# Kernel tuning notes

Measured on AMD Instinct MI355X. Metric: run time of the kernel, lower is better.

The kernel has to match this reference:

```python
import jax, jax.numpy as jnp
import numpy as np

B, C, NS, NT, H = 8, 256, 16384, 8192, 8
D = C // H  # 32
EPS_ATTN = 1e-6
EPS_LN = 1e-5


def _layernorm(x, g, b):
    m = jnp.mean(x, axis=-1, keepdims=True)
    v = jnp.mean((x - m) ** 2, axis=-1, keepdims=True)
    return (x - m) * jax.lax.rsqrt(v + EPS_LN) * g + b


def setup_inputs() -> dict:
    key = jax.random.key(0)
    ks = jax.random.split(key, 16)
    s = lambda fan_in: 1.0 / np.sqrt(fan_in)
    return {
        "search_feat": jax.random.normal(ks[0], (B, C, NS), jnp.float32),
        "search_xyz": jax.random.normal(ks[1], (B, NS, 3), jnp.float32),
        "template_feat": jax.random.normal(ks[2], (B, C, NT), jnp.float32),
        "template_xyz": jax.random.normal(ks[3], (B, NT, 3), jnp.float32),
        # pos_mlp: Linear(3, C) -> ReLU -> Linear(C, C); weights stored [in, out]
        "pos_w1": jax.random.uniform(ks[4], (3, C), jnp.float32, -s(3), s(3)),
        "pos_b1": jnp.zeros((C,), jnp.float32),
        "pos_w2": jax.random.uniform(ks[5], (C, C), jnp.float32, -s(C), s(C)),
        "pos_b2": jnp.zeros((C,), jnp.float32),
        "q_w": jax.random.uniform(ks[6], (C, C), jnp.float32, -s(C), s(C)),
        "k_w": jax.random.uniform(ks[7], (C, C), jnp.float32, -s(C), s(C)),
        "v_w": jax.random.uniform(ks[8], (C, C), jnp.float32, -s(C), s(C)),
        "merge_w": jax.random.uniform(ks[9], (C, C), jnp.float32, -s(C), s(C)),
        "mlp_w1": jax.random.uniform(ks[10], (2 * C, 2 * C), jnp.float32, -s(2 * C), s(2 * C)),
        "mlp_w2": jax.random.uniform(ks[11], (2 * C, C), jnp.float32, -s(2 * C), s(2 * C)),
        "ln1_g": jnp.ones((C,), jnp.float32),
        "ln1_b": jnp.zeros((C,), jnp.float32),
        "ln2_g": jnp.ones((C,), jnp.float32),
        "ln2_b": jnp.zeros((C,), jnp.float32),
    }


def _forward(search_feat, search_xyz, template_feat, template_xyz,
             pos_w1, pos_b1, pos_w2, pos_b2, q_w, k_w, v_w, merge_w,
             mlp_w1, mlp_w2, ln1_g, ln1_b, ln2_g, ln2_b):
    bs = search_feat.shape[0]
    sf = jnp.transpose(search_feat, (0, 2, 1))     # [B, Ns, C]
    tf = jnp.transpose(template_feat, (0, 2, 1))   # [B, Nt, C]
    # positional encoding added to template features before value projection
    pos = jax.nn.relu(template_xyz @ pos_w1 + pos_b1) @ pos_w2 + pos_b2
    tfp = tf + pos
    q = (sf @ q_w).reshape(bs, -1, H, D)    # [B, Ns, H, D]
    k = (tf @ k_w).reshape(bs, -1, H, D)    # [B, Nt, H, D]
    v = (tfp @ v_w).reshape(bs, -1, H, D)   # [B, Nt, H, D]
    # linear attention with elu+1 feature map
    Q = jax.nn.elu(q) + 1.0
    K = jax.nn.elu(k) + 1.0
    v_len = v.shape[1]
    v_scaled = v / v_len
    KV = jnp.einsum('nshd,nshv->nhdv', K, v_scaled)            # [B, H, D, D]
    Z = 1.0 / (jnp.einsum('nlhd,nhd->nlh', Q, K.sum(axis=1)) + EPS_ATTN)
    msg = jnp.einsum('nlhd,nhdv,nlh->nlhv', Q, KV, Z) * v_len  # [B, Ns, H, D]
    msg = msg.reshape(bs, -1, H * D) @ merge_w
    msg = _layernorm(msg, ln1_g, ln1_b)
    msg = jax.nn.relu(jnp.concatenate([sf, msg], axis=2) @ mlp_w1) @ mlp_w2
    msg = _layernorm(msg, ln2_g, ln2_b)
    return jnp.transpose(sf + msg, (0, 2, 1))  # [B, C, Ns]


def reference(search_feat, search_xyz, template_feat, template_xyz,
              pos_w1, pos_b1, pos_w2, pos_b2, q_w, k_w, v_w, merge_w,
              mlp_w1, mlp_w2, ln1_g, ln1_b, ln2_g, ln2_b):
    return _forward(search_feat, search_xyz, template_feat, template_xyz,
                    pos_w1, pos_b1, pos_w2, pos_b2, q_w, k_w, v_w, merge_w,
                    mlp_w1, mlp_w2, ln1_g, ln1_b, ln2_g, ln2_b)
```

## Files before the change

kernel.cpp:

```cpp
#include <hip/hip_runtime.h>
#include <math.h>

#define B_  8
#define C_  256
#define NS_ 16384
#define NT_ 8192
#define H_  8
#define D_  32
#define C2_ 512
#define NCH 4
#define KVZ_ (H_*D_*D_ + H_*D_)

typedef __attribute__((ext_vector_type(8))) short bf16x8;
typedef __attribute__((ext_vector_type(4))) short bf16x4;
typedef __attribute__((ext_vector_type(4))) float f32x4;

#define PIPE_TOP(N) do {                                              \
    asm volatile("s_waitcnt vmcnt(" #N ")" ::: "memory");             \
    asm volatile("s_barrier" ::: "memory");                           \
    __builtin_amdgcn_sched_barrier(0);                                \
} while (0)
#define PIPE_BOT() do {                                               \
    __builtin_amdgcn_sched_barrier(0);                                \
    asm volatile("s_waitcnt lgkmcnt(0)" ::: "memory");                \
    asm volatile("s_barrier" ::: "memory");                           \
} while (0)

__device__ __forceinline__ short f2bf(float f) {
    unsigned u = __float_as_uint(f);
    u = (u + 0x7fffu + ((u >> 16) & 1u)) >> 16;
    return (short)u;
}
__device__ __forceinline__ float bf2f(short s) {
    return __uint_as_float(((unsigned)(unsigned short)s) << 16);
}
__device__ __forceinline__ float2 bfpair(unsigned u) {
    float2 r;
    r.x = __uint_as_float(u << 16);
    r.y = __uint_as_float(u & 0xffff0000u);
    return r;
}
__device__ __forceinline__ void load_lds16(const void* g, void* l) {
    __builtin_amdgcn_global_load_lds(
        (const __attribute__((address_space(1))) unsigned int*)g,
        (__attribute__((address_space(3))) unsigned int*)l, 16, 0, 0);
}

__global__ __launch_bounds__(256)
void castT(const float* __restrict__ in, short* __restrict__ ob, int NLEN, int b0)
{
    __shared__ float tl[32][33];
    int g = blockIdx.z, gb = b0 + g;
    int n0 = blockIdx.x * 32, c0 = blockIdx.y * 32;
    int t = threadIdx.x, tr = t >> 5, tc = t & 31;
    #pragma unroll
    for (int i = 0; i < 4; ++i)
        tl[tr + 8*i][tc] = in[((size_t)gb*C_ + c0 + tr + 8*i)*NLEN + n0 + tc];
    __syncthreads();
    #pragma unroll
    for (int i = 0; i < 4; ++i)
        ob[((size_t)g*NLEN + n0 + tr + 8*i)*C_ + c0 + tc] = f2bf(tl[tc][tr + 8*i]);
}

struct WDesc { const float* src; int K; int N; int off; int ldo; };
struct WPack { WDesc d[7]; };

__global__ __launch_bounds__(256)
void wcast_all(WPack p, short* __restrict__ wt)
{
    __shared__ float tl[32][33];
    WDesc d = p.d[blockIdx.z];
    int kt = blockIdx.x * 32, nt = blockIdx.y * 32;
    if (kt >= d.K || nt >= d.N) return;
    int t = threadIdx.x, tr = t >> 5, tc = t & 31;
    #pragma unroll
    for (int i = 0; i < 4; ++i)
        tl[tr + 8*i][tc] = d.src[(size_t)(kt + tr + 8*i)*d.N + nt + tc];
    __syncthreads();
    short* o = wt + d.off;
    #pragma unroll
    for (int i = 0; i < 4; ++i)
        o[(size_t)(nt + tr + 8*i)*d.ldo + kt + tc] = f2bf(tl[tc][tr + 8*i]);
}

__global__ __launch_bounds__(256)
void fusew(short* __restrict__ wv2, const short* __restrict__ wp,
           const float* __restrict__ b2, const float* __restrict__ v_w,
           float* __restrict__ bv)
{
    int n = blockIdx.x, k = threadIdx.x;
    __shared__ float vrow[256];
    __shared__ float bred[256];
    vrow[k] = bf2f(wv2[(size_t)n*512 + k]);
    bred[k] = b2[k] * v_w[(size_t)k*C_ + n];
    __syncthreads();
    float s = 0.f;
    for (int m = 0; m < 256; ++m)
        s += vrow[m] * bf2f(wp[m*256 + k]);
    wv2[(size_t)n*512 + 256 + k] = f2bf(s);
    for (int off2 = 128; off2 > 0; off2 >>= 1) {
        __syncthreads();
        if (k < off2) bred[k] += bred[k + off2];
    }
    if (k == 0) bv[n] = bred[0];
}

__global__ __launch_bounds__(256)
void pos_h(const float* __restrict__ xyz, const float* __restrict__ w1,
           const float* __restrict__ b1, short* __restrict__ hb, int b0)
{
    int g = blockIdx.y, gb = b0 + g;
    int r0 = blockIdx.x * 16;
    int t = threadIdx.x;
    float w1x = w1[t], w1y = w1[C_ + t], w1z = w1[2*C_ + t], bb = b1[t];
    for (int r = 0; r < 16; ++r) {
        const float* p = xyz + ((size_t)gb*NT_ + r0 + r)*3;
        float h = fmaxf(p[0]*w1x + p[1]*w1y + p[2]*w1z + bb, 0.f);
        hb[((size_t)g*NT_ + r0 + r)*C_ + t] = f2bf(h);
    }
}

template<int EPI, int NF>
__global__ __launch_bounds__(256)
void gemm_bf16(const short* __restrict__ A0, int lda0,
               const short* __restrict__ A1, int lda1, int split,
               const short* __restrict__ Wt,
               const float* __restrict__ bias,
               short* __restrict__ outp,
               int M, int N, int K)
{
    __shared__ __align__(16) short As[3][128*32];
    __shared__ __align__(16) short Bs[3][NF*32*32];
    int g = blockIdx.z;
    int nbs = gridDim.x, Mb = gridDim.y;
    int nb, mb;
    if ((Mb & 7) == 0) {
        int lin = blockIdx.y * nbs + blockIdx.x;
        int xcd = lin & 7, j = lin >> 3;
        nb = (j % nbs) * (NF*32);
        mb = ((j / nbs) * 8 + xcd) * 128;
    } else {
        nb = blockIdx.x * (NF*32);
        mb = blockIdx.y * 128;
    }
    int t = threadIdx.x;
    int lane = t & 63;
    int w = t >> 6, wr = w >> 1, wc = w & 1;

    const short* A0g = A0 + (size_t)g*M*lda0;
    const short* A1g = A1 ? (A1 + (size_t)g*M*lda1) : A0;

    f32x4 acc[4][NF] = {};

    int r4 = t >> 2;
    int ch = t & 3;

    auto stage = [&](int buf, int kb) {
        const short* Ab; int lda, kc;
        if (kb < split) { Ab = A0g; lda = lda0; kc = kb; }
        else            { Ab = A1g; lda = lda1; kc = kb - split; }
        const short* as0 = Ab + (size_t)(mb + r4)*lda + kc + ch*8;
        load_lds16(as0,                   &As[buf][r4*32 + ch*8]);
        load_lds16(as0 + (size_t)64*lda,  &As[buf][(r4 + 64)*32 + ch*8]);
        #pragma unroll
        for (int i = 0; i < NF/2; ++i) {
            int row = r4 + 64*i;
            load_lds16(Wt + (size_t)(nb + row)*K + kb + ch*8, &Bs[buf][row*32 + ch*8]);
        }
    };

    int T = K >> 5;
    stage(0, 0);
    if (T > 1) stage(1, 32);
    int cur = 0;
    for (int tt = 0; tt < T; ++tt) {
        if (tt + 2 < T) {
            int st = (cur >= 1) ? cur - 1 : 2;
            stage(st, (tt + 2) << 5);
            PIPE_TOP(8);
        } else if (tt + 1 < T) {
            PIPE_TOP(4);
        } else {
            PIPE_TOP(0);
        }
        int kq = (lane >> 4) * 8;
        bf16x8 af[4], bfr[NF];
        #pragma unroll
        for (int m = 0; m < 4; ++m)
            af[m] = *(const bf16x8*)&As[cur][(wr*64 + m*16 + (lane & 15))*32 + kq];
        #pragma unroll
        for (int n = 0; n < NF; ++n)
            bfr[n] = *(const bf16x8*)&Bs[cur][(wc*(NF*16) + n*16 + (lane & 15))*32 + kq];
        #pragma unroll
        for (int m = 0; m < 4; ++m)
            #pragma unroll
            for (int n = 0; n < NF; ++n)
                acc[m][n] = __builtin_amdgcn_mfma_f32_16x16x32_bf16(
                    af[m], bfr[n], acc[m][n], 0, 0, 0);
        PIPE_BOT();
        cur = (cur == 2) ? 0 : cur + 1;
    }

    short* og = outp + (size_t)g*M*N;
    int rq = (lane >> 4) * 4;
    int cl = lane & 15;
    #pragma unroll
    for (int m = 0; m < 4; ++m) {
        #pragma unroll
        for (int r = 0; r < 4; ++r) {
            int row = mb + wr*64 + m*16 + rq + r;
            size_t ro = (size_t)row * N;
            #pragma unroll
            for (int n = 0; n < NF; ++n) {
                int col = nb + wc*(NF*16) + n*16 + cl;
                float v = acc[m][n][r];
                if constexpr (EPI == 1) v = fmaxf(v, 0.f);
                if constexpr (EPI == 2) v = (v > 0.f) ? (v + 1.f) : __expf(v);
                if constexpr (EPI == 4) v = v + bias[col];
                og[ro + col] = f2bf(v);
            }
        }
    }
}

__global__ __launch_bounds__(256)
void kv_kernel(const short* __restrict__ Kb, const short* __restrict__ Vb,
               float* __restrict__ kvz)
{
    __shared__ float SK[32][D_];
    __shared__ float SV[32][D_];
    int h = blockIdx.x, chk = blockIdx.y, g = blockIdx.z;
    int t = threadIdx.x;
    int d = t >> 3, v0 = (t & 7) * 4;
    int lr = t >> 3, lc = (t & 7) * 4;
    float acc[4] = {0.f, 0.f, 0.f, 0.f};
    float ksum = 0.f;
    int s0beg = chk * (NT_/NCH), s0end = s0beg + NT_/NCH;
    for (int s0 = s0beg; s0 < s0end; s0 += 32) {
        size_t off = ((size_t)g*NT_ + s0 + lr)*C_ + h*D_ + lc;
        uint2 ku = *(const uint2*)(Kb + off);
        uint2 vu = *(const uint2*)(Vb + off);
        float2 k0 = bfpair(ku.x), k1 = bfpair(ku.y);
        float2 w0 = bfpair(vu.x), w1 = bfpair(vu.y);
        SK[lr][lc] = k0.x; SK[lr][lc+1] = k0.y; SK[lr][lc+2] = k1.x; SK[lr][lc+3] = k1.y;
        SV[lr][lc] = w0.x; SV[lr][lc+1] = w0.y; SV[lr][lc+2] = w1.x; SV[lr][lc+3] = w1.y;
        __syncthreads();
        #pragma unroll
        for (int ss = 0; ss < 32; ++ss) {
            float kd = SK[ss][d];
            #pragma unroll
            for (int j = 0; j < 4; ++j) acc[j] += kd * SV[ss][v0 + j];
            ksum += kd;
        }
        __syncthreads();
    }
    float* KV = kvz + ((size_t)g*NCH + chk)*KVZ_;
    #pragma unroll
    for (int j = 0; j < 4; ++j) KV[h*D_*D_ + d*D_ + v0 + j] = acc[j];
    if ((t & 7) == 0) KV[H_*D_*D_ + h*D_ + d] = ksum;
}

__global__ __launch_bounds__(256)
void kvfin(const float* __restrict__ kvp, short* __restrict__ KVT,
           float* __restrict__ KSf)
{
    int g = blockIdx.x, t = threadIdx.x;
    const float* p = kvp + (size_t)g*NCH*KVZ_;
    for (int idx = t; idx < H_*D_*D_; idx += 256) {
        int h = idx >> 10, rem = idx & 1023, v = rem >> 5, d = rem & 31;
        float s = 0.f;
        #pragma unroll
        for (int c = 0; c < NCH; ++c) s += p[c*KVZ_ + h*1024 + d*32 + v];
        KVT[(size_t)g*8192 + h*1024 + v*32 + d] = f2bf(s);
    }
    {
        float s = 0.f;
        #pragma unroll
        for (int c = 0; c < NCH; ++c) s += p[c*KVZ_ + H_*D_*D_ + t];
        KSf[(size_t)g*256 + t] = s;
    }
}

__global__ __launch_bounds__(256)
void qam_kernel(const short* __restrict__ sfb, const short* __restrict__ wtq,
                const short* __restrict__ wtm, const short* __restrict__ KVT,
                const float* __restrict__ KSf,
                const float* __restrict__ ln1g, const float* __restrict__ ln1b,
                short* __restrict__ mrg)
{
    __shared__ short QT[64][264];
    __shared__ __align__(16) short stg[2*10240];
    __shared__ float sredS[4][64], sredQ[4][64];
    __shared__ float mrM[64], mrR[64];
    __shared__ float gbet[512];

    int g = blockIdx.y;
    int l0 = blockIdx.x * 64;
    int t = threadIdx.x;
    int lane = t & 63, w = t >> 6;
    int lx = lane & 15, ly = lane >> 4;

    gbet[t]       = ln1g[t];
    gbet[256 + t] = ln1b[t];

    const short* sfg = sfb + ((size_t)g*NS_ + l0)*C_;

    auto stage1 = [&](int buf, int kb) {
        short* As = stg + buf*10240;
        short* Bs = As + 2048;
        load_lds16(sfg + (size_t)(t>>2)*C_ + kb + (t&3)*8, &As[(t>>2)*32 + (t&3)*8]);
        #pragma unroll
        for (int i = 0; i < 4; ++i) {
            int row = (t>>2) + 64*i;
            load_lds16(wtq + (size_t)row*C_ + kb + (t&3)*8, &Bs[row*32 + (t&3)*8]);
        }
    };

    f32x4 acc[4][4] = {};
    stage1(0, 0);
    __syncthreads();
    int cur = 0;
    for (int kb = 0; kb < C_; kb += 32) {
        if (kb + 32 < C_) stage1(cur ^ 1, kb + 32);
        const short* As = stg + cur*10240;
        const short* Bs = As + 2048;
        bf16x8 af[4], bfv[4];
        #pragma unroll
        for (int m = 0; m < 4; ++m)
            af[m] = *(const bf16x8*)&Bs[(w*64 + m*16 + lx)*32 + ly*8];
        #pragma unroll
        for (int n = 0; n < 4; ++n)
            bfv[n] = *(const bf16x8*)&As[(n*16 + lx)*32 + ly*8];
        #pragma unroll
        for (int m = 0; m < 4; ++m)
            #pragma unroll
            for (int n = 0; n < 4; ++n)
                acc[m][n] = __builtin_amdgcn_mfma_f32_16x16x32_bf16(
                    af[m], bfv[n], acc[m][n], 0, 0, 0);
        __syncthreads();
        cur ^= 1;
    }
    #pragma unroll
    for (int m = 0; m < 4; ++m) {
        int c0 = w*64 + m*16 + ly*4;
        #pragma unroll
        for (int n = 0; n < 4; ++n) {
            bf16x4 pk;
            #pragma unroll
            for (int r = 0; r < 4; ++r) {
                float v = acc[m][n][r];
                pk[r] = f2bf((v > 0.f) ? (v + 1.f) : __expf(v));
            }
            *(bf16x4*)&QT[n*16 + lx][c0] = pk;
        }
    }
    __syncthreads();

    const short* kvg = KVT + (size_t)g*8192;
    bf16x8 bq[2][4];
    #pragma unroll
    for (int hh = 0; hh < 2; ++hh)
        #pragma unroll
        for (int n = 0; n < 4; ++n)
            bq[hh][n] = *(const bf16x8*)&QT[n*16 + lx][(2*w + hh)*32 + ly*8];
    float z[2][4];
    #pragma unroll
    for (int hh = 0; hh < 2; ++hh) {
        const float* kp = KSf + (size_t)g*256 + (2*w + hh)*32 + ly*8;
        float4 ka = *(const float4*)kp;
        float4 kb4 = *(const float4*)(kp + 4);
        float kr[8] = {ka.x, ka.y, ka.z, ka.w, kb4.x, kb4.y, kb4.z, kb4.w};
        #pragma unroll
        for (int n = 0; n < 4; ++n) {
            float s = 0.f;
            #pragma unroll
            for (int j = 0; j < 8; ++j) s += bf2f(bq[hh][n][j]) * kr[j];
            s += __shfl_xor(s, 16);
            s += __shfl_xor(s, 32);
            z[hh][n] = 1.f / (s + 1e-6f);
        }
    }
    f32x4 zero = {0.f, 0.f, 0.f, 0.f};
    f32x4 a2[4][4];
    #pragma unroll
    for (int m = 0; m < 4; ++m) {
        int h = 2*w + (m >> 1);
        bf16x8 afk = *(const bf16x8*)(kvg + ((size_t)h*1024 + ((m&1)*16 + lx)*32 + ly*8));
        #pragma unroll
        for (int n = 0; n < 4; ++n)
            a2[m][n] = __builtin_amdgcn_mfma_f32_16x16x32_bf16(
                afk, bq[m>>1][n], zero, 0, 0, 0);
    }
    #pragma unroll
    for (int m = 0; m < 4; ++m) {
        int c0 = w*64 + m*16 + ly*4;
        #pragma unroll
        for (int n = 0; n < 4; ++n) {
            bf16x4 pk;
            #pragma unroll
            for (int r = 0; r < 4; ++r)
                pk[r] = f2bf(a2[m][n][r] * z[m>>1][n]);
            *(bf16x4*)&QT[n*16 + lx][c0] = pk;
        }
    }
    __syncthreads();

    auto stage3 = [&](int buf, int kb) {
        short* Bs = stg + buf*10240 + 2048;
        #pragma unroll
        for (int i = 0; i < 4; ++i) {
            int row = (t>>2) + 64*i;
            load_lds16(wtm + (size_t)row*C_ + kb + (t&3)*8, &Bs[row*32 + (t&3)*8]);
        }
    };
    f32x4 acc3[4][4] = {};
    stage3(0, 0);
    __syncthreads();
    cur = 0;
    for (int kb = 0; kb < C_; kb += 32) {
        if (kb + 32 < C_) stage3(cur ^ 1, kb + 32);
        const short* Bs = stg + cur*10240 + 2048;
        bf16x8 af[4], bfv[4];
        #pragma unroll
        for (int m = 0; m < 4; ++m)
            af[m] = *(const bf16x8*)&Bs[(w*64 + m*16 + lx)*32 + ly*8];
        #pragma unroll
        for (int n = 0; n < 4; ++n)
            bfv[n] = *(const bf16x8*)&QT[n*16 + lx][kb + ly*8];
        #pragma unroll
        for (int m = 0; m < 4; ++m)
            #pragma unroll
            for (int n = 0; n < 4; ++n)
                acc3[m][n] = __builtin_amdgcn_mfma_f32_16x16x32_bf16(
                    af[m], bfv[n], acc3[m][n], 0, 0, 0);
        __syncthreads();
        cur ^= 1;
    }

    float sP[4] = {0,0,0,0}, qP[4] = {0,0,0,0};
    #pragma unroll
    for (int n = 0; n < 4; ++n)
        #pragma unroll
        for (int m = 0; m < 4; ++m)
            #pragma unroll
            for (int r = 0; r < 4; ++r) {
                float v = acc3[m][n][r];
                sP[n] += v; qP[n] += v*v;
            }
    #pragma unroll
    for (int n = 0; n < 4; ++n) {
        sP[n] += __shfl_xor(sP[n], 16); sP[n] += __shfl_xor(sP[n], 32);
        qP[n] += __shfl_xor(qP[n], 16); qP[n] += __shfl_xor(qP[n], 32);
    }
    if (ly == 0) {
        #pragma unroll
        for (int n = 0; n < 4; ++n) {
            sredS[w][n*16 + lx] = sP[n];
            sredQ[w][n*16 + lx] = qP[n];
        }
    }
    __syncthreads();
    if (t < 64) {
        float s = 0.f, q = 0.f;
        #pragma unroll
        for (int ww = 0; ww < 4; ++ww) { s += sredS[ww][t]; q += sredQ[ww][t]; }
        float m = s * (1.f/C_);
        mrM[t] = m;
        mrR[t] = rsqrtf(q*(1.f/C_) - m*m + 1e-5f);
    }
    __syncthreads();
    #pragma unroll
    for (int n = 0; n < 4; ++n) {
        float mn = mrM[n*16 + lx], rs = mrR[n*16 + lx];
        #pragma unroll
        for (int m = 0; m < 4; ++m) {
            int c0 = w*64 + m*16 + ly*4;
            bf16x4 pk;
            #pragma unroll
            for (int r = 0; r < 4; ++r) {
                int c = c0 + r;
                pk[r] = f2bf((acc3[m][n][r] - mn)*rs*gbet[c] + gbet[256 + c]);
            }
            *(bf16x4*)&QT[n*16 + lx][c0] = pk;
        }
    }
    __syncthreads();
    short* og = mrg + ((size_t)g*NS_ + l0)*C_;
    int row = t >> 2;
    #pragma unroll
    for (int i = 0; i < 8; ++i) {
        int chk = (t & 3) + 4*i;
        *(uint4*)(og + (size_t)row*C_ + chk*8) = *(const uint4*)&QT[row][chk*8];
    }
}

__global__ __launch_bounds__(256, 4)
void m2f_kernel(const short* __restrict__ hid, const short* __restrict__ wt2,
                const float* __restrict__ sfeat,
                const float* __restrict__ ln2g, const float* __restrict__ ln2b,
                float* __restrict__ out, int b0)
{
    __shared__ __align__(16) short sh[2*10240];
    __shared__ float sredS[4][64], sredQ[4][64];
    __shared__ float mrM[64], mrR[64];
    __shared__ float gbet[512];

    int g = blockIdx.y, gb = b0 + g;
    int l0 = blockIdx.x * 64;
    int t = threadIdx.x;
    int lane = t & 63, w = t >> 6;
    int lx = lane & 15, ly = lane >> 4;

    gbet[t]       = ln2g[t];
    gbet[256 + t] = ln2b[t];

    const short* hg = hid + ((size_t)g*NS_ + l0)*C2_;

    auto stage = [&](int buf, int kb) {
        short* As = sh + buf*10240;
        short* Bs = As + 8192;
        #pragma unroll
        for (int i = 0; i < 4; ++i) {
            int row = (t>>2) + 64*i;
            load_lds16(wt2 + (size_t)row*C2_ + kb + (t&3)*8, &As[row*32 + (t&3)*8]);
        }
        load_lds16(hg + (size_t)(t>>2)*C2_ + kb + (t&3)*8, &Bs[(t>>2)*32 + (t&3)*8]);
    };

    f32x4 acc[4][4] = {};
    stage(0, 0);
    __syncthreads();
    int cur = 0;
    for (int kb = 0; kb < C2_; kb += 32) {
        if (kb + 32 < C2_) stage(cur ^ 1, kb + 32);
        const short* As = sh + cur*10240;
        const short* Bs = As + 8192;
        bf16x8 af[4], bfv[4];
        #pragma unroll
        for (int m = 0; m < 4; ++m)
            af[m] = *(const bf16x8*)&As[(w*64 + m*16 + lx)*32 + ly*8];
        #pragma unroll
        for (int n = 0; n < 4; ++n)
            bfv[n] = *(const bf16x8*)&Bs[(n*16 + lx)*32 + ly*8];
        #pragma unroll
        for (int m = 0; m < 4; ++m)
            #pragma unroll
            for (int n = 0; n < 4; ++n)
                acc[m][n] = __builtin_amdgcn_mfma_f32_16x16x32_bf16(
                    af[m], bfv[n], acc[m][n], 0, 0, 0);
        __syncthreads();
        cur ^= 1;
    }

    float sP[4] = {0,0,0,0}, qP[4] = {0,0,0,0};
    #pragma unroll
    for (int n = 0; n < 4; ++n)
        #pragma unroll
        for (int m = 0; m < 4; ++m)
            #pragma unroll
            for (int r = 0; r < 4; ++r) {
                float v = acc[m][n][r];
                sP[n] += v; qP[n] += v*v;
            }
    #pragma unroll
    for (int n = 0; n < 4; ++n) {
        sP[n] += __shfl_xor(sP[n], 16); sP[n] += __shfl_xor(sP[n], 32);
        qP[n] += __shfl_xor(qP[n], 16); qP[n] += __shfl_xor(qP[n], 32);
    }
    if (ly == 0) {
        #pragma unroll
        for (int n = 0; n < 4; ++n) {
            sredS[w][n*16 + lx] = sP[n];
            sredQ[w][n*16 + lx] = qP[n];
        }
    }
    __syncthreads();
    if (t < 64) {
        float s = 0.f, q = 0.f;
        #pragma unroll
        for (int ww = 0; ww < 4; ++ww) { s += sredS[ww][t]; q += sredQ[ww][t]; }
        float m = s * (1.f/C_);
        mrM[t] = m;
        mrR[t] = rsqrtf(q*(1.f/C_) - m*m + 1e-5f);
    }
    __syncthreads();

    #pragma unroll
    for (int n = 0; n < 4; ++n) {
        int l = n*16 + lx;
        float mn = mrM[l], rs = mrR[l];
        #pragma unroll
        for (int m = 0; m < 4; ++m) {
            int c0 = w*64 + m*16 + ly*4;
            #pragma unroll
            for (int r = 0; r < 4; ++r)
                sh[l*258 + c0 + r] =
                    f2bf((acc[m][n][r] - mn)*rs*gbet[c0+r] + gbet[256 + c0 + r]);
        }
    }
    __syncthreads();

    int l = t & 63, cg = t >> 6;
    const float* sfp = sfeat + (size_t)gb*C_*NS_ + l0;
    float* op = out + (size_t)gb*C_*NS_ + l0;
    for (int ci = 0; ci < 64; ++ci) {
        int c = cg*64 + ci;
        size_t o = (size_t)c*NS_ + l;
        op[o] = sfp[o] + bf2f(sh[l*258 + c]);
    }
}

extern "C" void kernel_launch(void* const* d_in, const int* in_sizes, int n_in,
                              void* d_out, int out_size, void* d_ws, size_t ws_size,
                              hipStream_t stream)
{
    (void)in_sizes; (void)n_in; (void)out_size;
    const float* search_feat   = (const float*)d_in[0];
    const float* template_feat = (const float*)d_in[2];
    const float* template_xyz  = (const float*)d_in[3];
    const float* pos_w1  = (const float*)d_in[4];
    const float* pos_b1  = (const float*)d_in[5];
    const float* pos_w2  = (const float*)d_in[6];
    const float* pos_b2  = (const float*)d_in[7];
    const float* q_w     = (const float*)d_in[8];
    const float* k_w     = (const float*)d_in[9];
    const float* v_w     = (const float*)d_in[10];
    const float* merge_w = (const float*)d_in[11];
    const float* mlp_w1  = (const float*)d_in[12];
    const float* mlp_w2  = (const float*)d_in[13];
    const float* ln1_g   = (const float*)d_in[14];
    const float* ln1_b   = (const float*)d_in[15];
    const float* ln2_g   = (const float*)d_in[16];
    const float* ln2_b   = (const float*)d_in[17];
    float* out = (float*)d_out;

    const int W_Q = 0, W_K = 65536, W_M = 131072, W_P = 196608,
              W_1 = 262144, W_2 = 524288, W_V2 = 655360;
    const size_t wElems = 786432;

    size_t sfE = (size_t)NS_*C_, tfE = (size_t)NT_*C_;
    int G = 8;
    while (G > 1) {
        size_t shorts = (size_t)G*(4*sfE + tfE + 8192) + wElems;
        size_t bytes  = shorts*2 + (size_t)G*(NCH*KVZ_ + 256)*4 + 256*4 + 1024;
        if (bytes <= ws_size) break;
        G >>= 1;
    }

    short* wtb  = (short*)d_ws;
    short* sfb  = wtb  + wElems;
    short* tfb  = sfb  + (size_t)G*sfE;
    short* hid  = tfb  + (size_t)G*tfE;
    short* mrgb = hid  + (size_t)2*G*sfE;
    short* KVTb = mrgb + (size_t)G*sfE;
    float* kvpf = (float*)(KVTb + (size_t)G*8192);
    float* KSfb = kvpf + (size_t)G*NCH*KVZ_;
    float* bvf  = KSfb + (size_t)G*256;
    short* Kb = hid;
    short* Vb = hid + (size_t)G*tfE;
    short* hb = hid + (size_t)2*G*tfE;

    WPack pack;
    pack.d[0] = { q_w,     C_,  C_,  W_Q,  C_  };
    pack.d[1] = { k_w,     C_,  C_,  W_K,  C_  };
    pack.d[2] = { merge_w, C_,  C_,  W_M,  C_  };
    pack.d[3] = { pos_w2,  C_,  C_,  W_P,  C_  };
    pack.d[4] = { mlp_w1,  C2_, C2_, W_1,  C2_ };
    pack.d[5] = { mlp_w2,  C2_, C_,  W_2,  C2_ };
    pack.d[6] = { v_w,     C_,  C_,  W_V2, C2_ };
    wcast_all<<<dim3(16, 16, 7), 256, 0, stream>>>(pack, wtb);
    fusew<<<dim3(256), 256, 0, stream>>>(wtb + W_V2, wtb + W_P, pos_b2, v_w, bvf);

    for (int b0 = 0; b0 < B_; b0 += G) {
        castT<<<dim3(NS_/32, C_/32, G), 256, 0, stream>>>(search_feat, sfb, NS_, b0);
        castT<<<dim3(NT_/32, C_/32, G), 256, 0, stream>>>(template_feat, tfb, NT_, b0);
        pos_h<<<dim3(NT_/16, G), 256, 0, stream>>>(template_xyz, pos_w1, pos_b1, hb, b0);
        gemm_bf16<2,4><<<dim3(C_/128, NT_/128, G), 256, 0, stream>>>(
            tfb, C_, nullptr, 0, 1<<30, wtb + W_K, nullptr, Kb, NT_, C_, C_);
        gemm_bf16<4,4><<<dim3(C_/128, NT_/128, G), 256, 0, stream>>>(
            tfb, C_, hb, C_, C_, wtb + W_V2, bvf, Vb, NT_, C_, C2_);
        kv_kernel<<<dim3(H_, NCH, G), 256, 0, stream>>>(Kb, Vb, kvpf);
        kvfin<<<dim3(G), 256, 0, stream>>>(kvpf, KVTb, KSfb);
        qam_kernel<<<dim3(NS_/64, G), 256, 0, stream>>>(
            sfb, wtb + W_Q, wtb + W_M, KVTb, KSfb, ln1_g, ln1_b, mrgb);
        gemm_bf16<1,4><<<dim3(C2_/128, NS_/128, G), 256, 0, stream>>>(
            sfb, C_, mrgb, C_, C_, wtb + W_1, nullptr, hid, NS_, C2_, C2_);
        m2f_kernel<<<dim3(NS_/64, G), 256, 0, stream>>>(
            hid, wtb + W_2, search_feat, ln2_g, ln2_b, out, b0);
    }
}
```

Measured before the change: 526.4 us.

## Fuse MLP first GEMM with second GEMM and LayerNorm into one kernel

Replaces the separate mlp_w1 GEMM (which wrote the 512-wide hidden activation to global memory) and the m2f kernel with one 512-thread kernel. Each block computes its 64-row hidden tile in LDS with ReLU, then runs the second GEMM split over two K-halves across wave groups, reduces the partial sums through LDS, and applies LayerNorm plus the residual. This removes the global write and re-read of the hidden tensor and one launch. In exchange the kernel drops double buffering (load, sync, compute), uses much more LDS per block, which lowers occupancy, and reloads both weight matrices in every block.

```diff
diff --git a/kernel.cpp b/kernel.cpp
--- a/kernel.cpp
+++ b/kernel.cpp
@@ -494,16 +494,18 @@
     }
 }
 
-__global__ __launch_bounds__(256, 4)
-void m2f_kernel(const short* __restrict__ hid, const short* __restrict__ wt2,
-                const float* __restrict__ sfeat,
-                const float* __restrict__ ln2g, const float* __restrict__ ln2b,
-                float* __restrict__ out, int b0)
-{
-    __shared__ __align__(16) short sh[2*10240];
+__global__ __launch_bounds__(512)
+void mlpf_kernel(const short* __restrict__ sfb, const short* __restrict__ mrgb,
+                 const short* __restrict__ w1t, const short* __restrict__ w2t,
+                 const float* __restrict__ sfeat,
+                 const float* __restrict__ ln2g, const float* __restrict__ ln2b,
+                 float* __restrict__ out, int b0)
+{
+    __shared__ __align__(16) short stg[32768];
+    __shared__ __align__(16) short hidl[64*520];
+    __shared__ float gbet[512];
     __shared__ float sredS[4][64], sredQ[4][64];
     __shared__ float mrM[64], mrR[64];
-    __shared__ float gbet[512];
 
     int g = blockIdx.y, gb = b0 + g;
     int l0 = blockIdx.x * 64;
@@ -511,37 +513,34 @@
     int lane = t & 63, w = t >> 6;
     int lx = lane & 15, ly = lane >> 4;
 
-    gbet[t]       = ln2g[t];
-    gbet[256 + t] = ln2b[t];
-
-    const short* hg = hid + ((size_t)g*NS_ + l0)*C2_;
-
-    auto stage = [&](int buf, int kb) {
-        short* As = sh + buf*10240;
-        short* Bs = As + 8192;
+    gbet[t] = (t < 256) ? ln2g[t] : ln2b[t - 256];
+
+    const short* sfg = sfb  + ((size_t)g*NS_ + l0)*C_;
+    const short* mg  = mrgb + ((size_t)g*NS_ + l0)*C_;
+
+    f32x4 acc[4][4] = {};
+    for (int kb = 0; kb < C2_; kb += 32) {
         #pragma unroll
         for (int i = 0; i < 4; ++i) {
-            int row = (t>>2) + 64*i;
-            load_lds16(wt2 + (size_t)row*C2_ + kb + (t&3)*8, &As[row*32 + (t&3)*8]);
-        }
-        load_lds16(hg + (size_t)(t>>2)*C2_ + kb + (t&3)*8, &Bs[(t>>2)*32 + (t&3)*8]);
-    };
-
-    f32x4 acc[4][4] = {};
-    stage(0, 0);
-    __syncthreads();
-    int cur = 0;
-    for (int kb = 0; kb < C2_; kb += 32) {
-        if (kb + 32 < C2_) stage(cur ^ 1, kb + 32);
-        const short* As = sh + cur*10240;
-        const short* Bs = As + 8192;
+            int row = (t>>2) + 128*i;
+            load_lds16(w1t + (size_t)row*C2_ + kb + (t&3)*8,
+                       &stg[row*32 + (t&3)*8]);
+        }
+        if (t < 256) {
+            int l = t >> 2, ch = t & 3;
+            const short* src = (kb < C_)
+                ? (sfg + (size_t)l*C_ + kb + ch*8)
+                : (mg  + (size_t)l*C_ + (kb - C_) + ch*8);
+            load_lds16(src, &stg[16384 + l*32 + ch*8]);
+        }
+        __syncthreads();
         bf16x8 af[4], bfv[4];
         #pragma unroll
         for (int m = 0; m < 4; ++m)
-            af[m] = *(const bf16x8*)&As[(w*64 + m*16 + lx)*32 + ly*8];
+            af[m] = *(const bf16x8*)&stg[(w*64 + m*16 + lx)*32 + ly*8];
         #pragma unroll
         for (int n = 0; n < 4; ++n)
-            bfv[n] = *(const bf16x8*)&Bs[(n*16 + lx)*32 + ly*8];
+            bfv[n] = *(const bf16x8*)&stg[16384 + (n*16 + lx)*32 + ly*8];
         #pragma unroll
         for (int m = 0; m < 4; ++m)
             #pragma unroll
@@ -549,29 +548,86 @@
                 acc[m][n] = __builtin_amdgcn_mfma_f32_16x16x32_bf16(
                     af[m], bfv[n], acc[m][n], 0, 0, 0);
         __syncthreads();
-        cur ^= 1;
-    }
-
-    float sP[4] = {0,0,0,0}, qP[4] = {0,0,0,0};
-    #pragma unroll
-    for (int n = 0; n < 4; ++n)
-        #pragma unroll
-        for (int m = 0; m < 4; ++m)
-            #pragma unroll
-            for (int r = 0; r < 4; ++r) {
-                float v = acc[m][n][r];
-                sP[n] += v; qP[n] += v*v;
+    }
+    #pragma unroll
+    for (int n = 0; n < 4; ++n) {
+        int l = n*16 + lx;
+        #pragma unroll
+        for (int m = 0; m < 4; ++m) {
+            bf16x4 pk;
+            #pragma unroll
+            for (int r = 0; r < 4; ++r)
+                pk[r] = f2bf(fmaxf(acc[m][n][r], 0.f));
+            *(bf16x4*)&hidl[l*520 + w*64 + m*16 + ly*4] = pk;
+        }
+    }
+    __syncthreads();
+
+    int cq = w & 3, kh = w >> 2;
+    f32x4 acc3[4][4] = {};
+    for (int s = 0; s < 8; ++s) {
+        #pragma unroll
+        for (int i = 0; i < 4; ++i) {
+            int q = t + 512*i;
+            int tile = q >> 10, row = (q >> 2) & 255;
+            load_lds16(w2t + (size_t)row*C2_ + tile*C_ + s*32 + (t&3)*8,
+                       &stg[tile*8192 + row*32 + (t&3)*8]);
+        }
+        __syncthreads();
+        bf16x8 af[4], bfv[4];
+        #pragma unroll
+        for (int m = 0; m < 4; ++m)
+            af[m] = *(const bf16x8*)&stg[kh*8192 + (cq*64 + m*16 + lx)*32 + ly*8];
+        #pragma unroll
+        for (int n = 0; n < 4; ++n)
+            bfv[n] = *(const bf16x8*)&hidl[(n*16 + lx)*520 + kh*256 + s*32 + ly*8];
+        #pragma unroll
+        for (int m = 0; m < 4; ++m)
+            #pragma unroll
+            for (int n = 0; n < 4; ++n)
+                acc3[m][n] = __builtin_amdgcn_mfma_f32_16x16x32_bf16(
+                    af[m], bfv[n], acc3[m][n], 0, 0, 0);
+        __syncthreads();
+    }
+
+    float* dumpf = (float*)stg;
+    if (w >= 4) {
+        #pragma unroll
+        for (int m = 0; m < 4; ++m)
+            #pragma unroll
+            for (int n = 0; n < 4; ++n)
+                *(f32x4*)&dumpf[((w-4)*16 + m*4 + n)*256 + lane*4] = acc3[m][n];
+    }
+    __syncthreads();
+    if (w < 4) {
+        #pragma unroll
+        for (int m = 0; m < 4; ++m)
+            #pragma unroll
+            for (int n = 0; n < 4; ++n) {
+                f32x4 p = *(const f32x4*)&dumpf[(w*16 + m*4 + n)*256 + lane*4];
+                acc3[m][n] += p;
             }
-    #pragma unroll
-    for (int n = 0; n < 4; ++n) {
-        sP[n] += __shfl_xor(sP[n], 16); sP[n] += __shfl_xor(sP[n], 32);
-        qP[n] += __shfl_xor(qP[n], 16); qP[n] += __shfl_xor(qP[n], 32);
-    }
-    if (ly == 0) {
+        float sP[4] = {0,0,0,0}, qP[4] = {0,0,0,0};
+        #pragma unroll
+        for (int n = 0; n < 4; ++n)
+            #pragma unroll
+            for (int m = 0; m < 4; ++m)
+                #pragma unroll
+                for (int r = 0; r < 4; ++r) {
+                    float v = acc3[m][n][r];
+                    sP[n] += v; qP[n] += v*v;
+                }
         #pragma unroll
         for (int n = 0; n < 4; ++n) {
-            sredS[w][n*16 + lx] = sP[n];
-            sredQ[w][n*16 + lx] = qP[n];
+            sP[n] += __shfl_xor(sP[n], 16); sP[n] += __shfl_xor(sP[n], 32);
+            qP[n] += __shfl_xor(qP[n], 16); qP[n] += __shfl_xor(qP[n], 32);
+        }
+        if (ly == 0) {
+            #pragma unroll
+            for (int n = 0; n < 4; ++n) {
+                sredS[w][n*16 + lx] = sP[n];
+                sredQ[w][n*16 + lx] = qP[n];
+            }
         }
     }
     __syncthreads();
@@ -585,17 +641,20 @@
     }
     __syncthreads();
 
-    #pragma unroll
-    for (int n = 0; n < 4; ++n) {
-        int l = n*16 + lx;
-        float mn = mrM[l], rs = mrR[l];
-        #pragma unroll
-        for (int m = 0; m < 4; ++m) {
-            int c0 = w*64 + m*16 + ly*4;
-            #pragma unroll
-            for (int r = 0; r < 4; ++r)
-                sh[l*258 + c0 + r] =
-                    f2bf((acc[m][n][r] - mn)*rs*gbet[c0+r] + gbet[256 + c0 + r]);
+    short* os = stg;
+    if (w < 4) {
+        #pragma unroll
+        for (int n = 0; n < 4; ++n) {
+            int l = n*16 + lx;
+            float mn = mrM[l], rs = mrR[l];
+            #pragma unroll
+            for (int m = 0; m < 4; ++m) {
+                int c0 = w*64 + m*16 + ly*4;
+                #pragma unroll
+                for (int r = 0; r < 4; ++r)
+                    os[l*257 + c0 + r] =
+                        f2bf((acc3[m][n][r] - mn)*rs*gbet[c0+r] + gbet[256 + c0 + r]);
+            }
         }
     }
     __syncthreads();
@@ -603,10 +662,10 @@
     int l = t & 63, cg = t >> 6;
     const float* sfp = sfeat + (size_t)gb*C_*NS_ + l0;
     float* op = out + (size_t)gb*C_*NS_ + l0;
-    for (int ci = 0; ci < 64; ++ci) {
-        int c = cg*64 + ci;
+    for (int ci = 0; ci < 32; ++ci) {
+        int c = cg + 8*ci;
         size_t o = (size_t)c*NS_ + l;
-        op[o] = sfp[o] + bf2f(sh[l*258 + c]);
+        op[o] = sfp[o] + bf2f(os[l*257 + c]);
     }
 }
 
@@ -683,9 +742,7 @@
         kvfin<<<dim3(G), 256, 0, stream>>>(kvpf, KVTb, KSfb);
         qam_kernel<<<dim3(NS_/64, G), 256, 0, stream>>>(
             sfb, wtb + W_Q, wtb + W_M, KVTb, KSfb, ln1_g, ln1_b, mrgb);
-        gemm_bf16<1,4><<<dim3(C2_/128, NS_/128, G), 256, 0, stream>>>(
-            sfb, C_, mrgb, C_, C_, wtb + W_1, nullptr, hid, NS_, C2_, C2_);
-        m2f_kernel<<<dim3(NS_/64, G), 256, 0, stream>>>(
-            hid, wtb + W_2, search_feat, ln2_g, ln2_b, out, b0);
-    }
-}
+        mlpf_kernel<<<dim3(NS_/64, G), 512, 0, stream>>>(
+            sfb, mrgb, wtb + W_1, wtb + W_2, search_feat, ln2_g, ln2_b, out, b0);
+    }
+}
```

New measurement: 582.7 us. 1.11x slower.

## Widen final MLP-LN kernel to 128-row tiles with 512 threads

Applied to the files above, without the earlier changes.

The final GEMM+LayerNorm+residual kernel now processes 128 search points per block using 8 waves arranged 4x2, so each staged weight tile is reused across twice as many rows and the total weight traffic from L2 is halved. The output staging buffer uses an odd stride of 257 and an interleaved channel assignment, which should reduce LDS bank conflicts in the transposed write-out. In exchange, LDS use per block rises and the grid has half as many blocks, which may lower occupancy and latency hiding.

```diff
diff --git a/kernel.cpp b/kernel.cpp
--- a/kernel.cpp
+++ b/kernel.cpp
@@ -494,37 +494,41 @@
     }
 }
 
-__global__ __launch_bounds__(256, 4)
-void m2f_kernel(const short* __restrict__ hid, const short* __restrict__ wt2,
-                const float* __restrict__ sfeat,
-                const float* __restrict__ ln2g, const float* __restrict__ ln2b,
-                float* __restrict__ out, int b0)
-{
-    __shared__ __align__(16) short sh[2*10240];
-    __shared__ float sredS[4][64], sredQ[4][64];
-    __shared__ float mrM[64], mrR[64];
+__global__ __launch_bounds__(512)
+void m2f2_kernel(const short* __restrict__ hid, const short* __restrict__ wt2,
+                 const float* __restrict__ sfeat,
+                 const float* __restrict__ ln2g, const float* __restrict__ ln2b,
+                 float* __restrict__ out, int b0)
+{
+    __shared__ __align__(16) short stg[32896];
     __shared__ float gbet[512];
+    __shared__ float sredS[4][128], sredQ[4][128];
+    __shared__ float mrM[128], mrR[128];
 
     int g = blockIdx.y, gb = b0 + g;
-    int l0 = blockIdx.x * 64;
+    int l0 = blockIdx.x * 128;
     int t = threadIdx.x;
     int lane = t & 63, w = t >> 6;
     int lx = lane & 15, ly = lane >> 4;
-
-    gbet[t]       = ln2g[t];
-    gbet[256 + t] = ln2b[t];
+    int wc = w & 3, wl = w >> 2;
+
+    gbet[t] = (t < 256) ? ln2g[t] : ln2b[t - 256];
 
     const short* hg = hid + ((size_t)g*NS_ + l0)*C2_;
 
     auto stage = [&](int buf, int kb) {
-        short* As = sh + buf*10240;
+        short* As = stg + buf*12288;
         short* Bs = As + 8192;
         #pragma unroll
-        for (int i = 0; i < 4; ++i) {
-            int row = (t>>2) + 64*i;
-            load_lds16(wt2 + (size_t)row*C2_ + kb + (t&3)*8, &As[row*32 + (t&3)*8]);
-        }
-        load_lds16(hg + (size_t)(t>>2)*C2_ + kb + (t&3)*8, &Bs[(t>>2)*32 + (t&3)*8]);
+        for (int i = 0; i < 2; ++i) {
+            int q = t + 512*i;
+            int row = q >> 2, ch = q & 3;
+            load_lds16(wt2 + (size_t)row*C2_ + kb + ch*8, &As[row*32 + ch*8]);
+        }
+        {
+            int l = t >> 2, ch = t & 3;
+            load_lds16(hg + (size_t)l*C2_ + kb + ch*8, &Bs[l*32 + ch*8]);
+        }
     };
 
     f32x4 acc[4][4] = {};
@@ -533,15 +537,15 @@
     int cur = 0;
     for (int kb = 0; kb < C2_; kb += 32) {
         if (kb + 32 < C2_) stage(cur ^ 1, kb + 32);
-        const short* As = sh + cur*10240;
+        const short* As = stg + cur*12288;
         const short* Bs = As + 8192;
         bf16x8 af[4], bfv[4];
         #pragma unroll
         for (int m = 0; m < 4; ++m)
-            af[m] = *(const bf16x8*)&As[(w*64 + m*16 + lx)*32 + ly*8];
+            af[m] = *(const bf16x8*)&As[(wc*64 + m*16 + lx)*32 + ly*8];
         #pragma unroll
         for (int n = 0; n < 4; ++n)
-            bfv[n] = *(const bf16x8*)&Bs[(n*16 + lx)*32 + ly*8];
+            bfv[n] = *(const bf16x8*)&Bs[(wl*64 + n*16 + lx)*32 + ly*8];
         #pragma unroll
         for (int m = 0; m < 4; ++m)
             #pragma unroll
@@ -570,43 +574,44 @@
     if (ly == 0) {
         #pragma unroll
         for (int n = 0; n < 4; ++n) {
-            sredS[w][n*16 + lx] = sP[n];
-            sredQ[w][n*16 + lx] = qP[n];
-        }
-    }
-    __syncthreads();
-    if (t < 64) {
+            sredS[wc][wl*64 + n*16 + lx] = sP[n];
+            sredQ[wc][wl*64 + n*16 + lx] = qP[n];
+        }
+    }
+    __syncthreads();
+    if (t < 128) {
         float s = 0.f, q = 0.f;
         #pragma unroll
-        for (int ww = 0; ww < 4; ++ww) { s += sredS[ww][t]; q += sredQ[ww][t]; }
+        for (int p = 0; p < 4; ++p) { s += sredS[p][t]; q += sredQ[p][t]; }
         float m = s * (1.f/C_);
         mrM[t] = m;
         mrR[t] = rsqrtf(q*(1.f/C_) - m*m + 1e-5f);
     }
     __syncthreads();
 
+    short* os = stg;
     #pragma unroll
     for (int n = 0; n < 4; ++n) {
-        int l = n*16 + lx;
+        int l = wl*64 + n*16 + lx;
         float mn = mrM[l], rs = mrR[l];
         #pragma unroll
         for (int m = 0; m < 4; ++m) {
-            int c0 = w*64 + m*16 + ly*4;
+            int c0 = wc*64 + m*16 + ly*4;
             #pragma unroll
             for (int r = 0; r < 4; ++r)
-                sh[l*258 + c0 + r] =
+                os[l*257 + c0 + r] =
                     f2bf((acc[m][n][r] - mn)*rs*gbet[c0+r] + gbet[256 + c0 + r]);
         }
     }
     __syncthreads();
 
-    int l = t & 63, cg = t >> 6;
+    int l = t & 127, cg = t >> 7;
     const float* sfp = sfeat + (size_t)gb*C_*NS_ + l0;
     float* op = out + (size_t)gb*C_*NS_ + l0;
     for (int ci = 0; ci < 64; ++ci) {
-        int c = cg*64 + ci;
+        int c = cg + 4*ci;
         size_t o = (size_t)c*NS_ + l;
-        op[o] = sfp[o] + bf2f(sh[l*258 + c]);
+        op[o] = sfp[o] + bf2f(os[l*257 + c]);
     }
 }
 
@@ -685,7 +690,7 @@
             sfb, wtb + W_Q, wtb + W_M, KVTb, KSfb, ln1_g, ln1_b, mrgb);
         gemm_bf16<1,4><<<dim3(C2_/128, NS_/128, G), 256, 0, stream>>>(
             sfb, C_, mrgb, C_, C_, wtb + W_1, nullptr, hid, NS_, C2_, C2_);
-        m2f_kernel<<<dim3(NS_/64, G), 256, 0, stream>>>(
+        m2f2_kernel<<<dim3(NS_/128, G), 512, 0, stream>>>(
             hid, wtb + W_2, search_feat, ln2_g, ln2_b, out, b0);
     }
 }
```

New measurement: 530.5 us. About the same (+0.8%).
